# Kernel optimization log

Hardware: AMD Instinct MI355X
Metric: run time of the kernel (lower is better)

## Reference

```python
import jax, jax.numpy as jnp
import numpy as np

B, T, D = 4, 4096, 1024
C = 8.0  # RG_LRU constant c
LOGIT_LO = float(np.log(0.9 / 0.1))    # logit(0.9)
LOGIT_HI = float(np.log(0.999 / 0.001))  # logit(0.999)


def setup_inputs() -> dict:
    key = jax.random.key(0)
    ks = jax.random.split(key, 12)
    s = 1.0 / np.sqrt(D)
    z = lambda: jnp.zeros((D,), jnp.float32)
    return {
        "x": jax.random.normal(ks[0], (B, T, D), jnp.float32),
        "g1": jnp.ones((D,), jnp.float32),
        "g2": jnp.ones((D,), jnp.float32),
        # RecurrentBlock: shared linear, kernel-1 conv, output linear
        "W_lin": jax.random.normal(ks[1], (D, D), jnp.float32) * s, "b_lin": z(),
        "W_conv": jax.random.normal(ks[2], (D, D), jnp.float32) * s, "b_conv": z(),
        "W_lin2": jax.random.normal(ks[3], (D, D), jnp.float32) * s, "b_lin2": z(),
        # RG_LRU params
        "Wa": jax.random.normal(ks[4], (D, D), jnp.float32) * s, "ba": z(),
        "Wx": jax.random.normal(ks[5], (D, D), jnp.float32) * s, "bx": z(),
        "Lam": jax.random.uniform(ks[6], (D,), jnp.float32, LOGIT_LO, LOGIT_HI),
        # GatedMLPBlock
        "W1": jax.random.normal(ks[7], (D, D), jnp.float32) * s, "b1": z(),
        "W2": jax.random.normal(ks[8], (D, D), jnp.float32) * s, "b2": z(),
        "W3": jax.random.normal(ks[9], (D, D), jnp.float32) * s, "b3": z(),
    }


def rms_norm(x, g):
    # F.normalize(x, dim=-1) * sqrt(d) * g
    n = jnp.maximum(jnp.linalg.norm(x, axis=-1, keepdims=True), 1e-12)
    return (x / n) * (x.shape[-1] ** 0.5) * g


def rg_lru(x, Wa, ba, Wx, bx, Lam):
    # x: [B, T, D]
    rt = jax.nn.sigmoid(jnp.einsum('btd,hd->bth', x, Wa) + ba)
    it = jax.nn.sigmoid(jnp.einsum('btd,hd->bth', x, Wx) + bx)
    log_a = -jax.nn.softplus(-Lam)          # [D]
    a = jnp.exp(log_a * rt / C)             # [B, T, D]
    gated = jnp.sqrt(1.0 - a * a) * (it * x)

    def step(h, ag):
        at, gt = ag
        h = at * h + gt
        return h, h

    h0 = jnp.zeros((x.shape[0], x.shape[2]), x.dtype)
    _, hs = jax.lax.scan(step, h0, (jnp.swapaxes(a, 0, 1), jnp.swapaxes(gated, 0, 1)))
    return jnp.swapaxes(hs, 0, 1)           # [B, T, D]


def reference(x, g1, g2, W_lin, b_lin, W_conv, b_conv, W_lin2, b_lin2,
              Wa, ba, Wx, bx, Lam, W1, b1, W2, b2, W3, b3):
    residual = x
    xn = rms_norm(x, g1)

    # RecurrentBlock (note: same linear used for both branches, as in source)
    lin = xn @ W_lin.T + b_lin
    x_gel = jax.nn.gelu(lin, approximate=False)
    x_rg = lin @ W_conv.T + b_conv          # Conv1d kernel_size=1 == pointwise linear
    x_rg = rg_lru(x_rg, Wa, ba, Wx, bx, Lam)
    xr = (x_gel * x_rg) @ W_lin2.T + b_lin2

    residual = xr + residual
    xm = rms_norm(residual, g2)

    # GatedMLPBlock
    out = jax.nn.sigmoid(xm @ W1.T + b1)
    gate = jax.nn.gelu(out, approximate=False)
    combined = gate * (xm @ W2.T + b2)
    y = combined @ W3.T + b3
    return y + residual
```

## Files before the change

kernel.cpp:

```cpp
#include <hip/hip_runtime.h>
#include <cstdint>
#include <cstddef>

typedef unsigned short u16;
typedef __attribute__((ext_vector_type(8))) __bf16 bf16x8;
typedef __attribute__((ext_vector_type(4))) float f32x4;

#define DD 1024
#define MM 16384
#define NCH 64
#define CLEN 64
#define EPAD 136

__device__ __forceinline__ u16 f2b(float f) {
    uint32_t u = __float_as_uint(f);
    u += 0x7fffu + ((u >> 16) & 1u);
    return (u16)(u >> 16);
}
__device__ __forceinline__ float b2f(u16 v) {
    return __uint_as_float(((uint32_t)v) << 16);
}
__device__ __forceinline__ float sigmoid_f(float v) { return 1.f / (1.f + __expf(-v)); }
__device__ __forceinline__ float gelu_f(float v) {
    return 0.5f * v * (1.f + erff(v * 0.70710678118654752f));
}

__device__ __forceinline__ void glds16(const u16* g, u16* l) {
    __builtin_amdgcn_global_load_lds(
        (const __attribute__((address_space(1))) void*)g,
        (__attribute__((address_space(3))) void*)l, 16, 0, 0);
}

__device__ __forceinline__ void swiz(int l, int& mt, int& nt) {
    const int g = l >> 6, r = l & 63;
    mt = g * 8 + (r & 7);
    nt = r >> 3;
}

template <int MODE>
__global__ __launch_bounds__(256, 2)
void gemm_bt(const u16* __restrict__ A, const u16* __restrict__ Bw,
             const float* __restrict__ bias, const float* __restrict__ auxf,
             u16* __restrict__ outb, float* __restrict__ outf)
{
    const int K = DD, N = DD;
    __shared__ __align__(16) u16 smem[8704];
    u16* As = smem;
    u16* Bs = smem + 4096;

    int mt, nt; swiz(blockIdx.x, mt, nt);
    const int m0 = mt * 128, n0 = nt * 128;
    const int tid = threadIdx.x;
    const int wave = tid >> 6, lane = tid & 63;
    const int wm = (wave >> 1) * 64, wn = (wave & 1) * 64;
    const int lr = lane & 15, lq = lane >> 4;

    const int trow = tid >> 2, tcol = tid & 3;
    const int kswz = (tcol ^ ((trow >> 1) & 3)) * 8;
    const u16* Ag = A + (size_t)(m0 + trow) * K + kswz;
    const u16* Bg = Bw + (size_t)(n0 + trow) * K + kswz;
    u16* la0 = &As[tid * 8];
    u16* la1 = &As[tid * 8 + 2048];
    u16* lb0 = &Bs[tid * 8];
    u16* lb1 = &Bs[tid * 8 + 2048];

    f32x4 acc[4][4] = {};

    for (int k0 = 0; k0 < K; k0 += 32) {
        glds16(Ag + k0, la0);
        glds16(Ag + (size_t)64 * K + k0, la1);
        glds16(Bg + k0, lb0);
        glds16(Bg + (size_t)64 * K + k0, lb1);
        __syncthreads();

        bf16x8 av[4], bv[4];
        const int cs = (lq ^ ((lr >> 1) & 3)) * 8;
#pragma unroll
        for (int i = 0; i < 4; i++)
            av[i] = *(const bf16x8*)&As[(wm + i * 16 + lr) * 32 + cs];
#pragma unroll
        for (int j = 0; j < 4; j++)
            bv[j] = *(const bf16x8*)&Bs[(wn + j * 16 + lr) * 32 + cs];
#pragma unroll
        for (int i = 0; i < 4; i++)
#pragma unroll
            for (int j = 0; j < 4; j++)
                acc[i][j] = __builtin_amdgcn_mfma_f32_16x16x32_bf16(
                    av[i], bv[j], acc[i][j], 0, 0, 0);
        __syncthreads();
    }

    if constexpr (MODE == 0) {
        for (int half = 0; half < 2; half++) {
            __syncthreads();
            if (wm == half * 64) {
#pragma unroll
                for (int i = 0; i < 4; i++)
#pragma unroll
                    for (int j = 0; j < 4; j++) {
                        const int col = wn + j * 16 + lr;
                        const float bz = bias[n0 + col];
#pragma unroll
                        for (int p = 0; p < 4; p++)
                            smem[(i * 16 + lq * 4 + p) * EPAD + col] =
                                f2b(acc[i][j][p] + bz);
                    }
            }
            __syncthreads();
#pragma unroll
            for (int t = 0; t < 4; t++) {
                const int f = t * 256 + tid;
                const int row = f >> 4, c8 = (f & 15) * 8;
                *(uint4*)&outb[(size_t)(m0 + half * 64 + row) * N + n0 + c8] =
                    *(const uint4*)&smem[row * EPAD + c8];
            }
        }
    } else {
#pragma unroll
        for (int i = 0; i < 4; i++) {
            const int mrow = m0 + wm + i * 16 + lq * 4;
#pragma unroll
            for (int j = 0; j < 4; j++) {
                const int ncol = n0 + wn + j * 16 + lr;
                const float bz = bias[ncol];
#pragma unroll
                for (int p = 0; p < 4; p++) {
                    const size_t idx = (size_t)(mrow + p) * N + ncol;
                    outf[idx] = acc[i][j][p] + bz + auxf[idx];
                }
            }
        }
    }
}

template <int DMODE>
__global__ __launch_bounds__(256, 2)
void gemm_dual(const u16* __restrict__ A, const u16* __restrict__ B1,
               const u16* __restrict__ B2,
               const float* __restrict__ bias1, const float* __restrict__ bias2,
               u16* __restrict__ out1, u16* __restrict__ out2)
{
    const int K = DD, N = DD;
    __shared__ __align__(16) u16 smem[12288];
    u16* As = smem;
    u16* Bs1 = smem + 4096;
    u16* Bs2 = smem + 8192;

    int mt, nt; swiz(blockIdx.x, mt, nt);
    const int m0 = mt * 128, n0 = nt * 128;
    const int tid = threadIdx.x;
    const int wave = tid >> 6, lane = tid & 63;
    const int wm = (wave >> 1) * 64, wn = (wave & 1) * 64;
    const int lr = lane & 15, lq = lane >> 4;

    const int trow = tid >> 2, tcol = tid & 3;
    const int kswz = (tcol ^ ((trow >> 1) & 3)) * 8;
    const u16* Ag  = A  + (size_t)(m0 + trow) * K + kswz;
    const u16* B1g = B1 + (size_t)(n0 + trow) * K + kswz;
    const u16* B2g = B2 + (size_t)(n0 + trow) * K + kswz;
    u16* la0 = &As[tid * 8];
    u16* la1 = &As[tid * 8 + 2048];
    u16* lb10 = &Bs1[tid * 8];
    u16* lb11 = &Bs1[tid * 8 + 2048];
    u16* lb20 = &Bs2[tid * 8];
    u16* lb21 = &Bs2[tid * 8 + 2048];

    f32x4 acc1[4][4] = {}, acc2[4][4] = {};

    for (int k0 = 0; k0 < K; k0 += 32) {
        glds16(Ag + k0, la0);
        glds16(Ag + (size_t)64 * K + k0, la1);
        glds16(B1g + k0, lb10);
        glds16(B1g + (size_t)64 * K + k0, lb11);
        glds16(B2g + k0, lb20);
        glds16(B2g + (size_t)64 * K + k0, lb21);
        __syncthreads();

        bf16x8 av[4], bv1[4], bv2[4];
        const int cs = (lq ^ ((lr >> 1) & 3)) * 8;
#pragma unroll
        for (int i = 0; i < 4; i++)
            av[i] = *(const bf16x8*)&As[(wm + i * 16 + lr) * 32 + cs];
#pragma unroll
        for (int j = 0; j < 4; j++) {
            bv1[j] = *(const bf16x8*)&Bs1[(wn + j * 16 + lr) * 32 + cs];
            bv2[j] = *(const bf16x8*)&Bs2[(wn + j * 16 + lr) * 32 + cs];
        }
#pragma unroll
        for (int i = 0; i < 4; i++)
#pragma unroll
            for (int j = 0; j < 4; j++) {
                acc1[i][j] = __builtin_amdgcn_mfma_f32_16x16x32_bf16(
                    av[i], bv1[j], acc1[i][j], 0, 0, 0);
                acc2[i][j] = __builtin_amdgcn_mfma_f32_16x16x32_bf16(
                    av[i], bv2[j], acc2[i][j], 0, 0, 0);
            }
        __syncthreads();
    }

    if constexpr (DMODE == 0) {
#pragma unroll
        for (int o = 0; o < 2; o++) {
            const float* bz = o ? bias2 : bias1;
            u16* op = o ? out2 : out1;
            for (int half = 0; half < 2; half++) {
                __syncthreads();
                if (wm == half * 64) {
#pragma unroll
                    for (int i = 0; i < 4; i++)
#pragma unroll
                        for (int j = 0; j < 4; j++) {
                            const int col = wn + j * 16 + lr;
                            const float bb = bz[n0 + col];
#pragma unroll
                            for (int p = 0; p < 4; p++) {
                                const float v = (o ? acc2[i][j][p] : acc1[i][j][p]) + bb;
                                smem[(i * 16 + lq * 4 + p) * EPAD + col] = f2b(sigmoid_f(v));
                            }
                        }
                }
                __syncthreads();
#pragma unroll
                for (int t = 0; t < 4; t++) {
                    const int f = t * 256 + tid;
                    const int row = f >> 4, c8 = (f & 15) * 8;
                    *(uint4*)&op[(size_t)(m0 + half * 64 + row) * N + n0 + c8] =
                        *(const uint4*)&smem[row * EPAD + c8];
                }
            }
        }
    } else {
        for (int half = 0; half < 2; half++) {
            __syncthreads();
            if (wm == half * 64) {
#pragma unroll
                for (int i = 0; i < 4; i++)
#pragma unroll
                    for (int j = 0; j < 4; j++) {
                        const int col = wn + j * 16 + lr;
                        const float bb1 = bias1[n0 + col];
                        const float bb2 = bias2[n0 + col];
#pragma unroll
                        for (int p = 0; p < 4; p++) {
                            const float g = gelu_f(sigmoid_f(acc1[i][j][p] + bb1));
                            smem[(i * 16 + lq * 4 + p) * EPAD + col] =
                                f2b(g * (acc2[i][j][p] + bb2));
                        }
                    }
            }
            __syncthreads();
#pragma unroll
            for (int t = 0; t < 4; t++) {
                const int f = t * 256 + tid;
                const int row = f >> 4, c8 = (f & 15) * 8;
                *(uint4*)&out1[(size_t)(m0 + half * 64 + row) * N + n0 + c8] =
                    *(const uint4*)&smem[row * EPAD + c8];
            }
        }
    }
}

__global__ __launch_bounds__(256)
void rmsnorm_k(const float* __restrict__ x, const float* __restrict__ g,
               u16* __restrict__ out)
{
    const int row = blockIdx.x;
    const int t = threadIdx.x;
    const float4 v = ((const float4*)(x + (size_t)row * DD))[t];
    float ss = v.x * v.x + v.y * v.y + v.z * v.z + v.w * v.w;
#pragma unroll
    for (int o = 32; o > 0; o >>= 1) ss += __shfl_down(ss, o, 64);
    __shared__ float wsum[4];
    if ((t & 63) == 0) wsum[t >> 6] = ss;
    __syncthreads();
    const float tot = wsum[0] + wsum[1] + wsum[2] + wsum[3];
    const float sc = 32.0f * rsqrtf(fmaxf(tot, 1e-24f));
    const float4 gv = ((const float4*)g)[t];
    ushort4 o4;
    o4.x = f2b(v.x * sc * gv.x);
    o4.y = f2b(v.y * sc * gv.y);
    o4.z = f2b(v.z * sc * gv.z);
    o4.w = f2b(v.w * sc * gv.w);
    ((ushort4*)(out + (size_t)row * DD))[t] = o4;
}

struct W8 { const float* s[8]; };
__global__ __launch_bounds__(256)
void conv_w8(W8 w, u16* __restrict__ out)
{
    const float* in = w.s[blockIdx.y];
    u16* o = out + (size_t)blockIdx.y * DD * DD;
    const int i = (blockIdx.x * 256 + threadIdx.x) * 4;
    const float4 v = *(const float4*)(in + i);
    ushort4 r;
    r.x = f2b(v.x); r.y = f2b(v.y); r.z = f2b(v.z); r.w = f2b(v.w);
    *(ushort4*)(o + i) = r;
}

__global__ __launch_bounds__(256)
void scan_chunks(const u16* __restrict__ rt, const u16* __restrict__ it,
                 const u16* __restrict__ rg, const float* __restrict__ Lam,
                 float* __restrict__ P, float* __restrict__ Hl)
{
    const int d = blockIdx.x * 256 + threadIdx.x;
    const int c = blockIdx.y, b = blockIdx.z;
    const float k = -log1pf(__expf(-Lam[d])) * 0.125f;
    const size_t base = (((size_t)b * 4096) + (size_t)c * CLEN) * DD + d;
    float p = 1.f, h = 0.f;
#pragma unroll 4
    for (int t = 0; t < CLEN; t++) {
        const size_t ix = base + (size_t)t * DD;
        const float r = b2f(rt[ix]);
        const float i = b2f(it[ix]);
        const float xv = b2f(rg[ix]);
        const float a = __expf(k * r);
        const float g = sqrtf(fmaxf(1.f - a * a, 0.f)) * (i * xv);
        p *= a;
        h = fmaf(a, h, g);
    }
    const int o = (b * NCH + c) * DD + d;
    P[o] = p;
    Hl[o] = h;
}

__global__ __launch_bounds__(256)
void scan_carry(const float* __restrict__ P, const float* __restrict__ Hl,
                float* __restrict__ Cin)
{
    const int idx = blockIdx.x * 256 + threadIdx.x;
    const int b = idx >> 10, d = idx & 1023;
    float h = 0.f;
    for (int c = 0; c < NCH; c++) {
        const int o = (b * NCH + c) * DD + d;
        Cin[o] = h;
        h = fmaf(P[o], h, Hl[o]);
    }
}

__global__ __launch_bounds__(256)
void scan_apply(const u16* __restrict__ rt, const u16* __restrict__ it,
                const u16* __restrict__ rg, const u16* __restrict__ lin,
                const float* __restrict__ Lam, const float* __restrict__ Cin,
                u16* __restrict__ yin)
{
    const int d = blockIdx.x * 256 + threadIdx.x;
    const int c = blockIdx.y, b = blockIdx.z;
    const float k = -log1pf(__expf(-Lam[d])) * 0.125f;
    const size_t base = (((size_t)b * 4096) + (size_t)c * CLEN) * DD + d;
    float h = Cin[(b * NCH + c) * DD + d];
#pragma unroll 4
    for (int t = 0; t < CLEN; t++) {
        const size_t ix = base + (size_t)t * DD;
        const float r = b2f(rt[ix]);
        const float i = b2f(it[ix]);
        const float xv = b2f(rg[ix]);
        const float a = __expf(k * r);
        const float g = sqrtf(fmaxf(1.f - a * a, 0.f)) * (i * xv);
        h = fmaf(a, h, g);
        const float l = b2f(lin[ix]);
        yin[ix] = f2b(gelu_f(l) * h);
    }
}

extern "C" void kernel_launch(void* const* d_in, const int* in_sizes, int n_in,
                              void* d_out, int out_size, void* d_ws, size_t ws_size,
                              hipStream_t stream)
{
    const float* x      = (const float*)d_in[0];
    const float* g1     = (const float*)d_in[1];
    const float* g2     = (const float*)d_in[2];
    const float* W_lin  = (const float*)d_in[3];
    const float* b_lin  = (const float*)d_in[4];
    const float* W_conv = (const float*)d_in[5];
    const float* b_conv = (const float*)d_in[6];
    const float* W_lin2 = (const float*)d_in[7];
    const float* b_lin2 = (const float*)d_in[8];
    const float* Wa     = (const float*)d_in[9];
    const float* ba     = (const float*)d_in[10];
    const float* Wx     = (const float*)d_in[11];
    const float* bx     = (const float*)d_in[12];
    const float* Lam    = (const float*)d_in[13];
    const float* W1     = (const float*)d_in[14];
    const float* b1     = (const float*)d_in[15];
    const float* W2     = (const float*)d_in[16];
    const float* b2     = (const float*)d_in[17];
    const float* W3     = (const float*)d_in[18];
    const float* b3     = (const float*)d_in[19];
    float* out = (float*)d_out;

    char* p = (char*)d_ws;
    auto alloc = [&](size_t bytes) -> char* {
        char* q = p;
        p += (bytes + 255) & ~(size_t)255;
        return q;
    };
    const size_t MD = (size_t)MM * DD;
    u16* wball = (u16*)alloc((size_t)8 * DD * DD * 2);
    u16* t0 = (u16*)alloc(MD * 2);
    u16* t1 = (u16*)alloc(MD * 2);
    u16* t2 = (u16*)alloc(MD * 2);
    u16* t3 = (u16*)alloc(MD * 2);
    u16* t4 = (u16*)alloc(MD * 2);
    float* res2 = (float*)alloc(MD * 4);
    float* P   = (float*)alloc((size_t)4 * NCH * DD * 4);
    float* Hl  = (float*)alloc((size_t)4 * NCH * DD * 4);
    float* Cin = (float*)alloc((size_t)4 * NCH * DD * 4);

    W8 w8;
    w8.s[0] = W_lin; w8.s[1] = W_conv; w8.s[2] = Wa; w8.s[3] = Wx;
    w8.s[4] = W_lin2; w8.s[5] = W1; w8.s[6] = W2; w8.s[7] = W3;
    conv_w8<<<dim3(DD * DD / 1024, 8), 256, 0, stream>>>(w8, wball);
    u16* wbf[8];
    for (int i = 0; i < 8; i++) wbf[i] = wball + (size_t)i * DD * DD;

    const int gg = (MM / 128) * (DD / 128);
    const dim3 sg(DD / 256, NCH, 4);

    rmsnorm_k<<<MM, 256, 0, stream>>>(x, g1, t0);
    gemm_bt<0><<<gg, 256, 0, stream>>>(t0, wbf[0], b_lin, nullptr, t1, nullptr);
    gemm_bt<0><<<gg, 256, 0, stream>>>(t1, wbf[1], b_conv, nullptr, t2, nullptr);
    gemm_dual<0><<<gg, 256, 0, stream>>>(t2, wbf[2], wbf[3], ba, bx, t0, t3);
    scan_chunks<<<sg, 256, 0, stream>>>(t0, t3, t2, Lam, P, Hl);
    scan_carry<<<4096 / 256, 256, 0, stream>>>(P, Hl, Cin);
    scan_apply<<<sg, 256, 0, stream>>>(t0, t3, t2, t1, Lam, Cin, t4);
    gemm_bt<2><<<gg, 256, 0, stream>>>(t4, wbf[4], b_lin2, x, nullptr, res2);
    rmsnorm_k<<<MM, 256, 0, stream>>>(res2, g2, t0);
    gemm_dual<1><<<gg, 256, 0, stream>>>(t0, wbf[5], wbf[6], b1, b2, t2, nullptr);
    gemm_bt<2><<<gg, 256, 0, stream>>>(t2, wbf[7], b3, res2, nullptr, out);
}
```

Baseline: 654.6 us.

## Double-buffer LDS tiles in GEMM kernels to overlap global loads with MFMA

Both GEMM kernels now use two LDS buffers. The next K-tile is prefetched with global_load_lds while the current tile is consumed, and partial vmcnt waits plus raw barriers replace the two __syncthreads per iteration. The goal is to hide global memory latency behind the MFMA work. The cost is doubled LDS use (64KB and 96KB per block in the dual kernel), which may limit occupancy below the two blocks requested by launch bounds.

Measured after the change: 626.4 us. 1.05x faster.

```diff
diff --git a/kernel.cpp b/kernel.cpp
--- a/kernel.cpp
+++ b/kernel.cpp
@@ -44,9 +44,11 @@
              u16* __restrict__ outb, float* __restrict__ outf)
 {
     const int K = DD, N = DD;
-    __shared__ __align__(16) u16 smem[8704];
-    u16* As = smem;
-    u16* Bs = smem + 4096;
+    __shared__ __align__(16) u16 smem[16384];
+    u16* const As0 = smem;
+    u16* const Bs0 = smem + 4096;
+    u16* const As1 = smem + 8192;
+    u16* const Bs1 = smem + 12288;
 
     int mt, nt; swiz(blockIdx.x, mt, nt);
     const int m0 = mt * 128, n0 = nt * 128;
@@ -59,35 +61,47 @@
     const int kswz = (tcol ^ ((trow >> 1) & 3)) * 8;
     const u16* Ag = A + (size_t)(m0 + trow) * K + kswz;
     const u16* Bg = Bw + (size_t)(n0 + trow) * K + kswz;
-    u16* la0 = &As[tid * 8];
-    u16* la1 = &As[tid * 8 + 2048];
-    u16* lb0 = &Bs[tid * 8];
-    u16* lb1 = &Bs[tid * 8 + 2048];
+    const int st = tid * 8;
+    const int cs = (lq ^ ((lr >> 1) & 3)) * 8;
 
     f32x4 acc[4][4] = {};
 
+    glds16(Ag, As0 + st);
+    glds16(Ag + (size_t)64 * K, As0 + st + 2048);
+    glds16(Bg, Bs0 + st);
+    glds16(Bg + (size_t)64 * K, Bs0 + st + 2048);
+
+#pragma unroll 2
     for (int k0 = 0; k0 < K; k0 += 32) {
-        glds16(Ag + k0, la0);
-        glds16(Ag + (size_t)64 * K + k0, la1);
-        glds16(Bg + k0, lb0);
-        glds16(Bg + (size_t)64 * K + k0, lb1);
-        __syncthreads();
+        u16* const Ac = ((k0 >> 5) & 1) ? As1 : As0;
+        u16* const Bc = ((k0 >> 5) & 1) ? Bs1 : Bs0;
+        if (k0 + 32 < K) {
+            u16* const An = ((k0 >> 5) & 1) ? As0 : As1;
+            u16* const Bn = ((k0 >> 5) & 1) ? Bs0 : Bs1;
+            const int kn = k0 + 32;
+            glds16(Ag + kn, An + st);
+            glds16(Ag + (size_t)64 * K + kn, An + st + 2048);
+            glds16(Bg + kn, Bn + st);
+            glds16(Bg + (size_t)64 * K + kn, Bn + st + 2048);
+            asm volatile("s_waitcnt vmcnt(4)\ns_barrier" ::: "memory");
+        } else {
+            asm volatile("s_waitcnt vmcnt(0)\ns_barrier" ::: "memory");
+        }
 
         bf16x8 av[4], bv[4];
-        const int cs = (lq ^ ((lr >> 1) & 3)) * 8;
 #pragma unroll
         for (int i = 0; i < 4; i++)
-            av[i] = *(const bf16x8*)&As[(wm + i * 16 + lr) * 32 + cs];
+            av[i] = *(const bf16x8*)&Ac[(wm + i * 16 + lr) * 32 + cs];
 #pragma unroll
         for (int j = 0; j < 4; j++)
-            bv[j] = *(const bf16x8*)&Bs[(wn + j * 16 + lr) * 32 + cs];
+            bv[j] = *(const bf16x8*)&Bc[(wn + j * 16 + lr) * 32 + cs];
 #pragma unroll
         for (int i = 0; i < 4; i++)
 #pragma unroll
             for (int j = 0; j < 4; j++)
                 acc[i][j] = __builtin_amdgcn_mfma_f32_16x16x32_bf16(
                     av[i], bv[j], acc[i][j], 0, 0, 0);
-        __syncthreads();
+        asm volatile("s_barrier" ::: "memory");
     }
 
     if constexpr (MODE == 0) {
@@ -141,10 +155,13 @@
                u16* __restrict__ out1, u16* __restrict__ out2)
 {
     const int K = DD, N = DD;
-    __shared__ __align__(16) u16 smem[12288];
-    u16* As = smem;
-    u16* Bs1 = smem + 4096;
-    u16* Bs2 = smem + 8192;
+    __shared__ __align__(16) u16 smem[24576];
+    u16* const As0  = smem;
+    u16* const B1s0 = smem + 4096;
+    u16* const B2s0 = smem + 8192;
+    u16* const As1  = smem + 12288;
+    u16* const B1s1 = smem + 16384;
+    u16* const B2s1 = smem + 20480;
 
     int mt, nt; swiz(blockIdx.x, mt, nt);
     const int m0 = mt * 128, n0 = nt * 128;
@@ -158,33 +175,48 @@
     const u16* Ag  = A  + (size_t)(m0 + trow) * K + kswz;
     const u16* B1g = B1 + (size_t)(n0 + trow) * K + kswz;
     const u16* B2g = B2 + (size_t)(n0 + trow) * K + kswz;
-    u16* la0 = &As[tid * 8];
-    u16* la1 = &As[tid * 8 + 2048];
-    u16* lb10 = &Bs1[tid * 8];
-    u16* lb11 = &Bs1[tid * 8 + 2048];
-    u16* lb20 = &Bs2[tid * 8];
-    u16* lb21 = &Bs2[tid * 8 + 2048];
+    const int st = tid * 8;
+    const int cs = (lq ^ ((lr >> 1) & 3)) * 8;
 
     f32x4 acc1[4][4] = {}, acc2[4][4] = {};
 
+    glds16(Ag, As0 + st);
+    glds16(Ag + (size_t)64 * K, As0 + st + 2048);
+    glds16(B1g, B1s0 + st);
+    glds16(B1g + (size_t)64 * K, B1s0 + st + 2048);
+    glds16(B2g, B2s0 + st);
+    glds16(B2g + (size_t)64 * K, B2s0 + st + 2048);
+
+#pragma unroll 2
     for (int k0 = 0; k0 < K; k0 += 32) {
-        glds16(Ag + k0, la0);
-        glds16(Ag + (size_t)64 * K + k0, la1);
-        glds16(B1g + k0, lb10);
-        glds16(B1g + (size_t)64 * K + k0, lb11);
-        glds16(B2g + k0, lb20);
-        glds16(B2g + (size_t)64 * K + k0, lb21);
-        __syncthreads();
+        const int par = (k0 >> 5) & 1;
+        u16* const Ac  = par ? As1  : As0;
+        u16* const B1c = par ? B1s1 : B1s0;
+        u16* const B2c = par ? B2s1 : B2s0;
+        if (k0 + 32 < K) {
+            u16* const An  = par ? As0  : As1;
+            u16* const B1n = par ? B1s0 : B1s1;
+            u16* const B2n = par ? B2s0 : B2s1;
+            const int kn = k0 + 32;
+            glds16(Ag + kn, An + st);
+            glds16(Ag + (size_t)64 * K + kn, An + st + 2048);
+            glds16(B1g + kn, B1n + st);
+            glds16(B1g + (size_t)64 * K + kn, B1n + st + 2048);
+            glds16(B2g + kn, B2n + st);
+            glds16(B2g + (size_t)64 * K + kn, B2n + st + 2048);
+            asm volatile("s_waitcnt vmcnt(6)\ns_barrier" ::: "memory");
+        } else {
+            asm volatile("s_waitcnt vmcnt(0)\ns_barrier" ::: "memory");
+        }
 
         bf16x8 av[4], bv1[4], bv2[4];
-        const int cs = (lq ^ ((lr >> 1) & 3)) * 8;
 #pragma unroll
         for (int i = 0; i < 4; i++)
-            av[i] = *(const bf16x8*)&As[(wm + i * 16 + lr) * 32 + cs];
+            av[i] = *(const bf16x8*)&Ac[(wm + i * 16 + lr) * 32 + cs];
 #pragma unroll
         for (int j = 0; j < 4; j++) {
-            bv1[j] = *(const bf16x8*)&Bs1[(wn + j * 16 + lr) * 32 + cs];
-            bv2[j] = *(const bf16x8*)&Bs2[(wn + j * 16 + lr) * 32 + cs];
+            bv1[j] = *(const bf16x8*)&B1c[(wn + j * 16 + lr) * 32 + cs];
+            bv2[j] = *(const bf16x8*)&B2c[(wn + j * 16 + lr) * 32 + cs];
         }
 #pragma unroll
         for (int i = 0; i < 4; i++)
@@ -195,7 +227,7 @@
                 acc2[i][j] = __builtin_amdgcn_mfma_f32_16x16x32_bf16(
                     av[i], bv2[j], acc2[i][j], 0, 0, 0);
             }
-        __syncthreads();
+        asm volatile("s_barrier" ::: "memory");
     }
 
     if constexpr (DMODE == 0) {
```

## Fold conv linear into first linear via precomputed weight product and register-prefetch GEMM loads

Applied to the files above, without the earlier changes.

Precomputes W_conv·W_lin (and the combined bias) on device so that the lin and conv projections become one dual GEMM reading xn, instead of two chained GEMMs where the second depends on the first's output. This removes a full 16384x1024 GEMM pass plus its intermediate round-trip, at the cost of a small 1024^3 weight GEMM and a transpose per call. The conv branch now derives from unrounded xn products rather than the bf16-rounded lin, which shifts numerics slightly. Separately, the GEMM mainloops replace global_load_lds with register-staged prefetch of the next K tile, stored to LDS after the MFMAs, to overlap global latency with compute.

Measured after the change: 656.6 us. About the same (+0.3%).

```diff
diff --git a/kernel.cpp b/kernel.cpp
--- a/kernel.cpp
+++ b/kernel.cpp
@@ -25,12 +25,6 @@
     return 0.5f * v * (1.f + erff(v * 0.70710678118654752f));
 }
 
-__device__ __forceinline__ void glds16(const u16* g, u16* l) {
-    __builtin_amdgcn_global_load_lds(
-        (const __attribute__((address_space(1))) void*)g,
-        (__attribute__((address_space(3))) void*)l, 16, 0, 0);
-}
-
 __device__ __forceinline__ void swiz(int l, int& mt, int& nt) {
     const int g = l >> 6, r = l & 63;
     mt = g * 8 + (r & 7);
@@ -45,8 +39,8 @@
 {
     const int K = DD, N = DD;
     __shared__ __align__(16) u16 smem[8704];
-    u16* As = smem;
-    u16* Bs = smem + 4096;
+    u16* const As = smem;
+    u16* const Bs = smem + 4096;
 
     int mt, nt; swiz(blockIdx.x, mt, nt);
     const int m0 = mt * 128, n0 = nt * 128;
@@ -59,22 +53,34 @@
     const int kswz = (tcol ^ ((trow >> 1) & 3)) * 8;
     const u16* Ag = A + (size_t)(m0 + trow) * K + kswz;
     const u16* Bg = Bw + (size_t)(n0 + trow) * K + kswz;
-    u16* la0 = &As[tid * 8];
-    u16* la1 = &As[tid * 8 + 2048];
-    u16* lb0 = &Bs[tid * 8];
-    u16* lb1 = &Bs[tid * 8 + 2048];
+    const int st = tid * 8;
+    const int cs = (lq ^ ((lr >> 1) & 3)) * 8;
 
     f32x4 acc[4][4] = {};
 
+    {
+        const uint4 a0 = *(const uint4*)(Ag);
+        const uint4 a1 = *(const uint4*)(Ag + (size_t)64 * K);
+        const uint4 b0 = *(const uint4*)(Bg);
+        const uint4 b1 = *(const uint4*)(Bg + (size_t)64 * K);
+        *(uint4*)&As[st] = a0;
+        *(uint4*)&As[st + 2048] = a1;
+        *(uint4*)&Bs[st] = b0;
+        *(uint4*)&Bs[st + 2048] = b1;
+    }
+
     for (int k0 = 0; k0 < K; k0 += 32) {
-        glds16(Ag + k0, la0);
-        glds16(Ag + (size_t)64 * K + k0, la1);
-        glds16(Bg + k0, lb0);
-        glds16(Bg + (size_t)64 * K + k0, lb1);
-        __syncthreads();
+        const int kn = k0 + 32;
+        uint4 na0, na1, nb0, nb1;
+        if (kn < K) {
+            na0 = *(const uint4*)(Ag + kn);
+            na1 = *(const uint4*)(Ag + (size_t)64 * K + kn);
+            nb0 = *(const uint4*)(Bg + kn);
+            nb1 = *(const uint4*)(Bg + (size_t)64 * K + kn);
+        }
+        asm volatile("s_waitcnt lgkmcnt(0)\ns_barrier" ::: "memory");
 
         bf16x8 av[4], bv[4];
-        const int cs = (lq ^ ((lr >> 1) & 3)) * 8;
 #pragma unroll
         for (int i = 0; i < 4; i++)
             av[i] = *(const bf16x8*)&As[(wm + i * 16 + lr) * 32 + cs];
@@ -87,10 +93,32 @@
             for (int j = 0; j < 4; j++)
                 acc[i][j] = __builtin_amdgcn_mfma_f32_16x16x32_bf16(
                     av[i], bv[j], acc[i][j], 0, 0, 0);
-        __syncthreads();
-    }
-
-    if constexpr (MODE == 0) {
+
+        asm volatile("s_barrier" ::: "memory");
+        if (kn < K) {
+            *(uint4*)&As[st] = na0;
+            *(uint4*)&As[st + 2048] = na1;
+            *(uint4*)&Bs[st] = nb0;
+            *(uint4*)&Bs[st + 2048] = nb1;
+        }
+    }
+
+    if constexpr (MODE == 2) {
+#pragma unroll
+        for (int i = 0; i < 4; i++) {
+            const int mrow = m0 + wm + i * 16 + lq * 4;
+#pragma unroll
+            for (int j = 0; j < 4; j++) {
+                const int ncol = n0 + wn + j * 16 + lr;
+                const float bz = bias[ncol];
+#pragma unroll
+                for (int p = 0; p < 4; p++) {
+                    const size_t idx = (size_t)(mrow + p) * N + ncol;
+                    outf[idx] = acc[i][j][p] + bz + auxf[idx];
+                }
+            }
+        }
+    } else {
         for (int half = 0; half < 2; half++) {
             __syncthreads();
             if (wm == half * 64) {
@@ -99,11 +127,10 @@
 #pragma unroll
                     for (int j = 0; j < 4; j++) {
                         const int col = wn + j * 16 + lr;
-                        const float bz = bias[n0 + col];
 #pragma unroll
                         for (int p = 0; p < 4; p++)
                             smem[(i * 16 + lq * 4 + p) * EPAD + col] =
-                                f2b(acc[i][j][p] + bz);
+                                f2b(acc[i][j][p]);
                     }
             }
             __syncthreads();
@@ -113,21 +140,6 @@
                 const int row = f >> 4, c8 = (f & 15) * 8;
                 *(uint4*)&outb[(size_t)(m0 + half * 64 + row) * N + n0 + c8] =
                     *(const uint4*)&smem[row * EPAD + c8];
-            }
-        }
-    } else {
-#pragma unroll
-        for (int i = 0; i < 4; i++) {
-            const int mrow = m0 + wm + i * 16 + lq * 4;
-#pragma unroll
-            for (int j = 0; j < 4; j++) {
-                const int ncol = n0 + wn + j * 16 + lr;
-                const float bz = bias[ncol];
-#pragma unroll
-                for (int p = 0; p < 4; p++) {
-                    const size_t idx = (size_t)(mrow + p) * N + ncol;
-                    outf[idx] = acc[i][j][p] + bz + auxf[idx];
-                }
             }
         }
     }
@@ -142,9 +154,9 @@
 {
     const int K = DD, N = DD;
     __shared__ __align__(16) u16 smem[12288];
-    u16* As = smem;
-    u16* Bs1 = smem + 4096;
-    u16* Bs2 = smem + 8192;
+    u16* const As  = smem;
+    u16* const B1s = smem + 4096;
+    u16* const B2s = smem + 8192;
 
     int mt, nt; swiz(blockIdx.x, mt, nt);
     const int m0 = mt * 128, n0 = nt * 128;
@@ -158,33 +170,47 @@
     const u16* Ag  = A  + (size_t)(m0 + trow) * K + kswz;
     const u16* B1g = B1 + (size_t)(n0 + trow) * K + kswz;
     const u16* B2g = B2 + (size_t)(n0 + trow) * K + kswz;
-    u16* la0 = &As[tid * 8];
-    u16* la1 = &As[tid * 8 + 2048];
-    u16* lb10 = &Bs1[tid * 8];
-    u16* lb11 = &Bs1[tid * 8 + 2048];
-    u16* lb20 = &Bs2[tid * 8];
-    u16* lb21 = &Bs2[tid * 8 + 2048];
+    const int st = tid * 8;
+    const int cs = (lq ^ ((lr >> 1) & 3)) * 8;
 
     f32x4 acc1[4][4] = {}, acc2[4][4] = {};
 
+    {
+        const uint4 a0 = *(const uint4*)(Ag);
+        const uint4 a1 = *(const uint4*)(Ag + (size_t)64 * K);
+        const uint4 p0 = *(const uint4*)(B1g);
+        const uint4 p1 = *(const uint4*)(B1g + (size_t)64 * K);
+        const uint4 q0 = *(const uint4*)(B2g);
+        const uint4 q1 = *(const uint4*)(B2g + (size_t)64 * K);
+        *(uint4*)&As[st] = a0;
+        *(uint4*)&As[st + 2048] = a1;
+        *(uint4*)&B1s[st] = p0;
+        *(uint4*)&B1s[st + 2048] = p1;
+        *(uint4*)&B2s[st] = q0;
+        *(uint4*)&B2s[st + 2048] = q1;
+    }
+
     for (int k0 = 0; k0 < K; k0 += 32) {
-        glds16(Ag + k0, la0);
-        glds16(Ag + (size_t)64 * K + k0, la1);
-        glds16(B1g + k0, lb10);
-        glds16(B1g + (size_t)64 * K + k0, lb11);
-        glds16(B2g + k0, lb20);
-        glds16(B2g + (size_t)64 * K + k0, lb21);
-        __syncthreads();
+        const int kn = k0 + 32;
+        uint4 na0, na1, nb0, nb1, nc0, nc1;
+        if (kn < K) {
+            na0 = *(const uint4*)(Ag + kn);
+            na1 = *(const uint4*)(Ag + (size_t)64 * K + kn);
+            nb0 = *(const uint4*)(B1g + kn);
+            nb1 = *(const uint4*)(B1g + (size_t)64 * K + kn);
+            nc0 = *(const uint4*)(B2g + kn);
+            nc1 = *(const uint4*)(B2g + (size_t)64 * K + kn);
+        }
+        asm volatile("s_waitcnt lgkmcnt(0)\ns_barrier" ::: "memory");
 
         bf16x8 av[4], bv1[4], bv2[4];
-        const int cs = (lq ^ ((lr >> 1) & 3)) * 8;
 #pragma unroll
         for (int i = 0; i < 4; i++)
             av[i] = *(const bf16x8*)&As[(wm + i * 16 + lr) * 32 + cs];
 #pragma unroll
         for (int j = 0; j < 4; j++) {
-            bv1[j] = *(const bf16x8*)&Bs1[(wn + j * 16 + lr) * 32 + cs];
-            bv2[j] = *(const bf16x8*)&Bs2[(wn + j * 16 + lr) * 32 + cs];
+            bv1[j] = *(const bf16x8*)&B1s[(wn + j * 16 + lr) * 32 + cs];
+            bv2[j] = *(const bf16x8*)&B2s[(wn + j * 16 + lr) * 32 + cs];
         }
 #pragma unroll
         for (int i = 0; i < 4; i++)
@@ -195,10 +221,18 @@
                 acc2[i][j] = __builtin_amdgcn_mfma_f32_16x16x32_bf16(
                     av[i], bv2[j], acc2[i][j], 0, 0, 0);
             }
-        __syncthreads();
-    }
-
-    if constexpr (DMODE == 0) {
+        asm volatile("s_barrier" ::: "memory");
+        if (kn < K) {
+            *(uint4*)&As[st] = na0;
+            *(uint4*)&As[st + 2048] = na1;
+            *(uint4*)&B1s[st] = nb0;
+            *(uint4*)&B1s[st + 2048] = nb1;
+            *(uint4*)&B2s[st] = nc0;
+            *(uint4*)&B2s[st + 2048] = nc1;
+        }
+    }
+
+    if constexpr (DMODE == 0 || DMODE == 2) {
 #pragma unroll
         for (int o = 0; o < 2; o++) {
             const float* bz = o ? bias2 : bias1;
@@ -214,8 +248,9 @@
                             const float bb = bz[n0 + col];
 #pragma unroll
                             for (int p = 0; p < 4; p++) {
-                                const float v = (o ? acc2[i][j][p] : acc1[i][j][p]) + bb;
-                                smem[(i * 16 + lq * 4 + p) * EPAD + col] = f2b(sigmoid_f(v));
+                                float v = (o ? acc2[i][j][p] : acc1[i][j][p]) + bb;
+                                if constexpr (DMODE == 0) v = sigmoid_f(v);
+                                smem[(i * 16 + lq * 4 + p) * EPAD + col] = f2b(v);
                             }
                         }
                 }
@@ -295,6 +330,47 @@
     ushort4 r;
     r.x = f2b(v.x); r.y = f2b(v.y); r.z = f2b(v.z); r.w = f2b(v.w);
     *(ushort4*)(o + i) = r;
+}
+
+__global__ __launch_bounds__(256)
+void trans_k(const float* __restrict__ in, u16* __restrict__ out)
+{
+    __shared__ float tl[64][65];
+    const int k0 = blockIdx.x * 64, d0 = blockIdx.y * 64;
+    const int t = threadIdx.x, tr = t >> 4, tc = t & 15;
+#pragma unroll
+    for (int i = 0; i < 4; i++) {
+        const int r = tr + i * 16;
+        const float4 v = *(const float4*)(in + (size_t)(k0 + r) * DD + d0 + tc * 4);
+        tl[r][tc * 4 + 0] = v.x; tl[r][tc * 4 + 1] = v.y;
+        tl[r][tc * 4 + 2] = v.z; tl[r][tc * 4 + 3] = v.w;
+    }
+    __syncthreads();
+#pragma unroll
+    for (int i = 0; i < 4; i++) {
+        const int r = tr + i * 16;
+        ushort4 o;
+        o.x = f2b(tl[tc * 4 + 0][r]);
+        o.y = f2b(tl[tc * 4 + 1][r]);
+        o.z = f2b(tl[tc * 4 + 2][r]);
+        o.w = f2b(tl[tc * 4 + 3][r]);
+        *(ushort4*)(out + (size_t)(d0 + r) * DD + k0 + tc * 4) = o;
+    }
+}
+
+__global__ __launch_bounds__(256)
+void bias_cl_k(const float* __restrict__ Wc, const float* __restrict__ bl,
+               const float* __restrict__ bc, float* __restrict__ out)
+{
+    const int n = blockIdx.x * 4 + (threadIdx.x >> 6);
+    const int lane = threadIdx.x & 63;
+    float s = 0.f;
+#pragma unroll
+    for (int i = 0; i < 16; i++)
+        s += Wc[(size_t)n * DD + lane + i * 64] * bl[lane + i * 64];
+#pragma unroll
+    for (int o = 32; o > 0; o >>= 1) s += __shfl_down(s, o, 64);
+    if (lane == 0) out[n] = s + bc[n];
 }
 
 __global__ __launch_bounds__(256)
@@ -396,6 +472,9 @@
     };
     const size_t MD = (size_t)MM * DD;
     u16* wball = (u16*)alloc((size_t)8 * DD * DD * 2);
+    u16* wlinT = (u16*)alloc((size_t)DD * DD * 2);
+    u16* Wcl   = (u16*)alloc((size_t)DD * DD * 2);
+    float* bcl = (float*)alloc((size_t)DD * 4);
     u16* t0 = (u16*)alloc(MD * 2);
     u16* t1 = (u16*)alloc(MD * 2);
     u16* t2 = (u16*)alloc(MD * 2);
@@ -413,12 +492,15 @@
     u16* wbf[8];
     for (int i = 0; i < 8; i++) wbf[i] = wball + (size_t)i * DD * DD;
 
+    trans_k<<<dim3(16, 16), 256, 0, stream>>>(W_lin, wlinT);
+    gemm_bt<6><<<64, 256, 0, stream>>>(wbf[1], wlinT, nullptr, nullptr, Wcl, nullptr);
+    bias_cl_k<<<DD / 4, 256, 0, stream>>>(W_conv, b_lin, b_conv, bcl);
+
     const int gg = (MM / 128) * (DD / 128);
     const dim3 sg(DD / 256, NCH, 4);
 
     rmsnorm_k<<<MM, 256, 0, stream>>>(x, g1, t0);
-    gemm_bt<0><<<gg, 256, 0, stream>>>(t0, wbf[0], b_lin, nullptr, t1, nullptr);
-    gemm_bt<0><<<gg, 256, 0, stream>>>(t1, wbf[1], b_conv, nullptr, t2, nullptr);
+    gemm_dual<2><<<gg, 256, 0, stream>>>(t0, wbf[0], Wcl, b_lin, bcl, t1, t2);
     gemm_dual<0><<<gg, 256, 0, stream>>>(t2, wbf[2], wbf[3], ba, bx, t0, t3);
     scan_chunks<<<sg, 256, 0, stream>>>(t0, t3, t2, Lam, P, Hl);
     scan_carry<<<4096 / 256, 256, 0, stream>>>(P, Hl, Cin);
```
